# Optimization experiments

Measured on AMD Instinct MI355X. Metric: run time of the kernel, lower is better.

Reference implementation:

```python
import jax, jax.numpy as jnp
import numpy as np

B, S, D, H, V, C = 4, 2048, 1024, 16, 32000, 10
FFN_DIM = 2 * D
HD = D // H
SCALE = float(np.sqrt(HD))


def _posenc(seq, d):
    pos = jnp.arange(seq, dtype=jnp.float32)[:, None]
    div = jnp.exp(jnp.arange(0, d, 2, dtype=jnp.float32) * (-np.log(10000.0) / d))
    pe = jnp.zeros((seq, d), dtype=jnp.float32)
    pe = pe.at[:, 0::2].set(jnp.sin(pos * div))
    pe = pe.at[:, 1::2].set(jnp.cos(pos * div))
    return pe


def _layernorm(x, g, b, eps=1e-5):
    mu = jnp.mean(x, axis=-1, keepdims=True)
    var = jnp.mean(jnp.square(x - mu), axis=-1, keepdims=True)
    return (x - mu) * jax.lax.rsqrt(var + eps) * g + b


def setup_inputs() -> dict:
    key = jax.random.key(0)
    ks = jax.random.split(key, 10)
    x_ids = jax.random.randint(ks[0], (B, S), 0, V, dtype=jnp.int64 if jax.config.jax_enable_x64 else jnp.int32)
    mask = jnp.ones((B, S), dtype=jnp.int32)
    emb = (jax.random.normal(ks[1], (V, D), jnp.float32) * 0.02).at[0].set(0.0)  # padding_idx=0
    qkv_w = jax.random.normal(ks[2], (3 * D, D), jnp.float32) * 0.02
    fc_w = jax.random.normal(ks[3], (D, D), jnp.float32) * 0.02
    fc_b = jnp.zeros((D,), jnp.float32)
    ln1_g = jnp.ones((D,), jnp.float32); ln1_b = jnp.zeros((D,), jnp.float32)
    ffn_w1 = jax.random.normal(ks[4], (FFN_DIM, D), jnp.float32) * 0.02
    ffn_b1 = jnp.zeros((FFN_DIM,), jnp.float32)
    ffn_w2 = jax.random.normal(ks[5], (D, FFN_DIM), jnp.float32) * 0.02
    ffn_b2 = jnp.zeros((D,), jnp.float32)
    ln2_g = jnp.ones((D,), jnp.float32); ln2_b = jnp.zeros((D,), jnp.float32)
    pr_w1 = jax.random.normal(ks[6], (D, D), jnp.float32) * 0.02
    pr_b1 = jnp.zeros((D,), jnp.float32)
    pr_w2 = jax.random.normal(ks[7], (C, D), jnp.float32) * 0.02
    pr_b2 = jnp.zeros((C,), jnp.float32)
    return dict(x_ids=x_ids, mask=mask, emb=emb, qkv_w=qkv_w, fc_w=fc_w, fc_b=fc_b,
                ln1_g=ln1_g, ln1_b=ln1_b, ffn_w1=ffn_w1, ffn_b1=ffn_b1,
                ffn_w2=ffn_w2, ffn_b2=ffn_b2, ln2_g=ln2_g, ln2_b=ln2_b,
                pr_w1=pr_w1, pr_b1=pr_b1, pr_w2=pr_w2, pr_b2=pr_b2)


def reference(x_ids, mask, emb, qkv_w, fc_w, fc_b, ln1_g, ln1_b,
              ffn_w1, ffn_b1, ffn_w2, ffn_b2, ln2_g, ln2_b,
              pr_w1, pr_b1, pr_w2, pr_b2):
    # embedding + absolute positional encoding
    x = emb[x_ids] + _posenc(S, D)  # [B,S,D]
    residual = x
    # multi-head attention (dropout is identity at eval)
    qkv = jnp.einsum('bsd,ed->bse', x, qkv_w)  # [B,S,3D]
    q, k, v = jnp.split(qkv, 3, axis=-1)
    q = q.reshape(B, S, H, HD)
    k = k.reshape(B, S, H, HD)
    v = v.reshape(B, S, H, HD)
    attn = jnp.einsum('bqhd,bkhd->bhqk', q, k) / SCALE  # [B,H,S,S]
    attn = jnp.where(mask[:, None, None, :] == 0, -jnp.inf, attn)
    attn = jax.nn.softmax(attn, axis=-1)
    o = jnp.einsum('bhqk,bkhd->bqhd', attn, v).reshape(B, S, D)
    o = jnp.einsum('bsd,ed->bse', o, fc_w) + fc_b
    x = _layernorm(o + residual, ln1_g, ln1_b)
    # FFN block (residual + LayerNorm inside)
    h = jax.nn.gelu(jnp.einsum('bsd,fd->bsf', x, ffn_w1) + ffn_b1, approximate=False)
    h = jnp.einsum('bsf,df->bsd', h, ffn_w2) + ffn_b2
    x = _layernorm(h + x, ln2_g, ln2_b)
    # masked max-pool over sequence
    x = jnp.where(mask[:, :, None] == 0, -jnp.inf, x).max(axis=1)  # [B,D]
    # prediction head
    h = jax.nn.gelu(x @ pr_w1.T + pr_b1, approximate=False)
    logits = h @ pr_w2.T + pr_b2  # [B,C]
    return logits
```

## Files before the change

### kernel.cpp

```cpp
#include <hip/hip_runtime.h>
#include <math.h>

#define B_   4
#define S_   2048
#define D_   1024
#define H_   16
#define HD_  64
#define C_   10
#define FFN_ 2048
#define M_   (B_ * S_)
#define D3_  (3 * D_)

typedef unsigned short u16;
typedef __bf16 bf16x8 __attribute__((ext_vector_type(8)));
typedef float  f32x4  __attribute__((ext_vector_type(4)));

#define EXPSCL 0.18033688011112042f

__device__ __forceinline__ u16 f2bf(float f) {
  union { float f; unsigned u; } x; x.f = f;
  unsigned r = x.u + 0x7fffu + ((x.u >> 16) & 1u);
  return (u16)(r >> 16);
}
__device__ __forceinline__ unsigned cvtpk(float lo, float hi) {
  unsigned r;
  asm("v_cvt_pk_bf16_f32 %0, %1, %2" : "=v"(r) : "v"(lo), "v"(hi));
  return r;
}
__device__ __forceinline__ float gelu_f(float x) {
  return 0.5f * x * (1.f + erff(x * 0.70710678118654752440f));
}
__device__ __forceinline__ void gload_lds16(const void* g, void* l) {
  __builtin_amdgcn_global_load_lds(
      (const __attribute__((address_space(1))) unsigned int*)g,
      (__attribute__((address_space(3))) unsigned int*)l, 16, 0, 0);
}
__device__ __forceinline__ bf16x8 ldsfrag(const u16* buf, int rowbase, int fr, int kb) {
  return *(const bf16x8*)&buf[(rowbase + fr) * 64 + ((kb ^ (fr & 7)) << 3)];
}

#define CV0 786432
#define CV1 262144
#define CV2 524288
#define CV3 524288
__global__ __launch_bounds__(256) void cvt4_kernel(const float* __restrict__ s0,
                                                   const float* __restrict__ s1,
                                                   const float* __restrict__ s2,
                                                   const float* __restrict__ s3,
                                                   u16* __restrict__ d0,
                                                   u16* __restrict__ d1,
                                                   u16* __restrict__ d2,
                                                   u16* __restrict__ d3) {
  int v = blockIdx.x * 256 + threadIdx.x;
  const float* s; u16* d;
  if (v < CV0) { s = s0; d = d0; }
  else if (v < CV0 + CV1) { s = s1; d = d1; v -= CV0; }
  else if (v < CV0 + CV1 + CV2) { s = s2; d = d2; v -= CV0 + CV1; }
  else { s = s3; d = d3; v -= CV0 + CV1 + CV2; }
  const int i = v * 4;
  f32x4 x = *(const f32x4*)&s[i];
  ushort4 o;
  o.x = f2bf(x[0]); o.y = f2bf(x[1]); o.z = f2bf(x[2]); o.w = f2bf(x[3]);
  *(ushort4*)&d[i] = o;
}

__global__ __launch_bounds__(256) void embed_kernel(const int* __restrict__ ids,
                                                    const float* __restrict__ emb,
                                                    float* __restrict__ resid,
                                                    u16* __restrict__ xb) {
  const int m  = blockIdx.x;
  const int s  = m & (S_ - 1);
  const int id = ids[m];
  const int d0 = threadIdx.x * 4;
#pragma unroll
  for (int k = 0; k < 4; ++k) {
    const int d   = d0 + k;
    const float e = emb[(size_t)id * D_ + d];
    const float fr  = expf((float)(d & ~1) * (-9.210340371976184f / 1024.0f));
    const float ang = (float)s * fr;
    const float pe  = (d & 1) ? cosf(ang) : sinf(ang);
    const float v   = e + pe;
    resid[(size_t)m * D_ + d] = v;
    xb[(size_t)m * D_ + d]    = f2bf(v);
  }
}

template <int BIAS, int GELU, int OUTBF, int QSCALE>
__global__ __launch_bounds__(256) void gemm_bt(const u16* __restrict__ A,
                                               const u16* __restrict__ W,
                                               const float* __restrict__ bias,
                                               float* __restrict__ outf,
                                               u16* __restrict__ outb,
                                               int M, int N, int K) {
  __shared__ u16 As[128 * 64];
  __shared__ u16 Bs[128 * 64];
  const int tid  = threadIdx.x;
  const int lane = tid & 63;
  const int w    = tid >> 6;
  const int bx   = blockIdx.x, by = blockIdx.y;
  const int l3   = lane >> 3;
  const int sb   = (lane & 7) ^ l3;
  const u16* Ag0 = A + (size_t)(by * 128 + w * 32 + l3) * K + sb * 8;
  const u16* Wg0 = W + (size_t)(bx * 128 + w * 32 + l3) * K + sb * 8;

  f32x4 acc[4][4] = {};
  const int wr  = (w & 1) * 64;
  const int wc  = (w >> 1) * 64;
  const int fr  = lane & 15;
  const int fq  = lane >> 4;

  for (int kt = 0; kt < K; kt += 64) {
#pragma unroll
    for (int c = 0; c < 4; ++c) {
      gload_lds16(Ag0 + (size_t)(c * 8) * K + kt, &As[(w * 32 + c * 8) * 64]);
      gload_lds16(Wg0 + (size_t)(c * 8) * K + kt, &Bs[(w * 32 + c * 8) * 64]);
    }
    __syncthreads();
#pragma unroll
    for (int ks = 0; ks < 2; ++ks) {
      const int kb = ks * 4 + fq;
      bf16x8 af[4], bfr[4];
#pragma unroll
      for (int i = 0; i < 4; ++i) af[i] = ldsfrag(As, wr + i * 16, fr, kb);
#pragma unroll
      for (int j = 0; j < 4; ++j) bfr[j] = ldsfrag(Bs, wc + j * 16, fr, kb);
#pragma unroll
      for (int i = 0; i < 4; ++i)
#pragma unroll
        for (int j = 0; j < 4; ++j)
          acc[i][j] = __builtin_amdgcn_mfma_f32_16x16x32_bf16(bfr[j], af[i], acc[i][j], 0, 0, 0);
    }
    __syncthreads();
  }

  const float qs = (QSCALE && bx < 8) ? EXPSCL : 1.f;
#pragma unroll
  for (int i = 0; i < 4; ++i) {
    const int m = by * 128 + wr + i * 16 + fr;
#pragma unroll
    for (int j = 0; j < 4; ++j) {
      const int nb = bx * 128 + wc + j * 16 + fq * 4;
      f32x4 v = acc[i][j];
      if (BIAS) v += *(const f32x4*)&bias[nb];
      if (GELU) {
        v[0] = gelu_f(v[0]); v[1] = gelu_f(v[1]);
        v[2] = gelu_f(v[2]); v[3] = gelu_f(v[3]);
      }
      if (QSCALE) v *= qs;
      if (OUTBF) {
        ushort4 pk;
        pk.x = f2bf(v[0]); pk.y = f2bf(v[1]); pk.z = f2bf(v[2]); pk.w = f2bf(v[3]);
        *(ushort4*)&outb[(size_t)m * N + nb] = pk;
      } else {
        *(f32x4*)&outf[(size_t)m * N + nb] = v;
      }
    }
  }
}

__global__ __launch_bounds__(256) void vtrans_kernel(const u16* __restrict__ qkv,
                                                     u16* __restrict__ vt) {
  __shared__ u16 t[64 * 65];
  const int tid = threadIdx.x;
  const int st = blockIdx.x, h = blockIdx.y, b = blockIdx.z;
  {
    const int r = tid & 63, cg = tid >> 6;
    const u16* src = qkv + (size_t)(b * S_ + st * 64 + r) * D3_ + 2 * D_ + h * 64 + cg * 16;
    union { uint4 q; u16 s[8]; } a, c;
    a.q = *(const uint4*)src;
    c.q = *(const uint4*)(src + 8);
    u16* dl = &t[r * 65 + cg * 16];
#pragma unroll
    for (int k = 0; k < 8; ++k) { dl[k] = a.s[k]; dl[8 + k] = c.s[k]; }
  }
  __syncthreads();
  const int d = tid >> 2, sq = tid & 3;
  union { uint4 q[2]; u16 s[16]; } o;
#pragma unroll
  for (int k = 0; k < 16; ++k) o.s[k] = t[(sq * 16 + k) * 65 + d];
  u16* dst = vt + ((size_t)((b * H_ + h) * 64 + d)) * S_ + st * 64 + sq * 16;
  *(uint4*)dst = o.q[0];
  *(uint4*)(dst + 8) = o.q[1];
}

__global__ __launch_bounds__(256) void attn_mfma_kernel(const u16* __restrict__ qkv,
                                                        const u16* __restrict__ vt,
                                                        const int* __restrict__ mask,
                                                        u16* __restrict__ attno) {
  __shared__ u16 Ks[64 * 64];
  __shared__ u16 Vts[64 * 64];
  __shared__ u16 Ps[4][32 * 64];
  const int tid = threadIdx.x, lane = tid & 63, w = tid >> 6;
  const int qt = blockIdx.x, h = blockIdx.y, b = blockIdx.z;
  const int l3 = lane >> 3;
  const int sb = (lane & 7) ^ l3;
  const int fr = lane & 15, fq = lane >> 4;
  u16* PsFlat = &Ps[0][0];

  {
    const u16* qbase = qkv + (size_t)(b * S_ + qt * 128 + w * 32) * D3_ + h * 64 + sb * 8;
#pragma unroll
    for (int c = 0; c < 4; ++c)
      gload_lds16(qbase + (size_t)(c * 8 + l3) * D3_, &PsFlat[(w * 32 + c * 8) * 64]);
  }

  bool ALLV;
  {
    const int4* mp = (const int4*)&mask[b * S_];
    int mv = 1;
#pragma unroll
    for (int t = 0; t < 8; ++t) {
      const int4 m4 = mp[t * 64 + lane];
      mv &= (m4.x != 0) & (m4.y != 0) & (m4.z != 0) & (m4.w != 0);
    }
    ALLV = (__ballot(mv != 0) == ~0ull);
  }

  __syncthreads();

  bf16x8 qf[2][2];
#pragma unroll
  for (int ks = 0; ks < 2; ++ks)
#pragma unroll
    for (int i = 0; i < 2; ++i)
      qf[ks][i] = ldsfrag(PsFlat, w * 32 + i * 16, fr, ks * 4 + fq);

  __syncthreads();

  float l_st[2] = {0.f, 0.f};
  f32x4 ot[4][2] = {};
  u16* PsW = Ps[w];

  for (int kt = 0; kt < S_ / 64; ++kt) {
    {
      const u16* kbase = qkv + (size_t)(b * S_ + kt * 64 + w * 16) * D3_ + D_ + h * 64 + sb * 8;
      gload_lds16(kbase + (size_t)l3 * D3_, &Ks[(w * 16) * 64]);
      gload_lds16(kbase + (size_t)(8 + l3) * D3_, &Ks[(w * 16 + 8) * 64]);
      const u16* vbase = vt + ((size_t)((b * H_ + h) * 64 + w * 16)) * S_ + kt * 64 + sb * 8;
      gload_lds16(vbase + (size_t)l3 * S_, &Vts[(w * 16) * 64]);
      gload_lds16(vbase + (size_t)(8 + l3) * S_, &Vts[(w * 16 + 8) * 64]);
    }
    __syncthreads();

    f32x4 sf[4][2] = {};
#pragma unroll
    for (int ks = 0; ks < 2; ++ks) {
      const int kb = ks * 4 + fq;
      __builtin_amdgcn_s_setprio(1);
#pragma unroll
      for (int r4 = 0; r4 < 4; ++r4) {
        bf16x8 kf = ldsfrag(Ks, r4 * 16, fr, kb);
        sf[r4][0] = __builtin_amdgcn_mfma_f32_16x16x32_bf16(kf, qf[ks][0], sf[r4][0], 0, 0, 0);
        sf[r4][1] = __builtin_amdgcn_mfma_f32_16x16x32_bf16(kf, qf[ks][1], sf[r4][1], 0, 0, 0);
      }
      __builtin_amdgcn_s_setprio(0);
    }
    if (!ALLV) {
#pragma unroll
      for (int r4 = 0; r4 < 4; ++r4) {
        const int4 mm = *(const int4*)&mask[b * S_ + kt * 64 + r4 * 16 + fq * 4];
        f32x4 vb;
        vb[0] = mm.x ? 0.f : -1e30f;
        vb[1] = mm.y ? 0.f : -1e30f;
        vb[2] = mm.z ? 0.f : -1e30f;
        vb[3] = mm.w ? 0.f : -1e30f;
        sf[r4][0] += vb;
        sf[r4][1] += vb;
      }
    }

#pragma unroll
    for (int i = 0; i < 2; ++i) {
      const int prow = i * 16 + fr;
      u16* pw = PsW + prow * 64;
      float sum = l_st[i];
#pragma unroll
      for (int r4 = 0; r4 < 4; ++r4) {
        const float p0 = __builtin_exp2f(sf[r4][i][0]);
        const float p1 = __builtin_exp2f(sf[r4][i][1]);
        const float p2 = __builtin_exp2f(sf[r4][i][2]);
        const float p3 = __builtin_exp2f(sf[r4][i][3]);
        sum += (p0 + p1) + (p2 + p3);
        const int bk0 = 2 * r4 + (fq >> 1);
        const int off = ((bk0 ^ (prow & 7)) << 3) + ((fq & 1) << 2);
        uint2 pk; pk.x = cvtpk(p0, p1); pk.y = cvtpk(p2, p3);
        *(uint2*)&pw[off] = pk;
      }
      l_st[i] = sum;
    }
    asm volatile("s_waitcnt lgkmcnt(0)" ::: "memory");

#pragma unroll
    for (int ks = 0; ks < 2; ++ks) {
      const int kb = ks * 4 + fq;
      bf16x8 pf0 = ldsfrag(PsW, 0, fr, kb);
      bf16x8 pf1 = ldsfrag(PsW, 16, fr, kb);
      __builtin_amdgcn_s_setprio(1);
#pragma unroll
      for (int db = 0; db < 4; ++db) {
        bf16x8 vf = ldsfrag(Vts, db * 16, fr, kb);
        ot[db][0] = __builtin_amdgcn_mfma_f32_16x16x32_bf16(vf, pf0, ot[db][0], 0, 0, 0);
        ot[db][1] = __builtin_amdgcn_mfma_f32_16x16x32_bf16(vf, pf1, ot[db][1], 0, 0, 0);
      }
      __builtin_amdgcn_s_setprio(0);
    }
    __syncthreads();
  }

#pragma unroll
  for (int i = 0; i < 2; ++i) {
    float l = l_st[i];
    l += __shfl_xor(l, 16);
    l += __shfl_xor(l, 32);
    const float inv = (l > 0.f) ? 1.f / l : 0.f;
    const int qrow = qt * 128 + w * 32 + i * 16 + fr;
    u16* dst = attno + (size_t)(b * S_ + qrow) * D_ + h * 64 + fq * 4;
#pragma unroll
    for (int db = 0; db < 4; ++db) {
      ushort4 pk;
      pk.x = f2bf(ot[db][i][0] * inv);
      pk.y = f2bf(ot[db][i][1] * inv);
      pk.z = f2bf(ot[db][i][2] * inv);
      pk.w = f2bf(ot[db][i][3] * inv);
      *(ushort4*)&dst[db * 16] = pk;
    }
  }
}

template <int WRITEB>
__global__ __launch_bounds__(256) void ln_kernel(const float* __restrict__ a,
                                                 const float* __restrict__ res,
                                                 const float* __restrict__ g,
                                                 const float* __restrict__ be,
                                                 float* __restrict__ outf,
                                                 u16* __restrict__ outb) {
  const int row = blockIdx.x, tid = threadIdx.x;
  const int lane = tid & 63, w = tid >> 6;
  const size_t base = (size_t)row * D_ + tid * 4;
  const f32x4 va = *(const f32x4*)(a + base);
  const f32x4 vr = *(const f32x4*)(res + base);
  const f32x4 v  = va + vr;
  float s = v[0] + v[1] + v[2] + v[3];
#pragma unroll
  for (int o = 32; o > 0; o >>= 1) s += __shfl_xor(s, o);
  __shared__ float red[8];
  if (lane == 0) red[w] = s;
  __syncthreads();
  const float mu = (red[0] + red[1] + red[2] + red[3]) * (1.f / D_);
  const f32x4 d = v - mu;
  float s2 = d[0] * d[0] + d[1] * d[1] + d[2] * d[2] + d[3] * d[3];
#pragma unroll
  for (int o = 32; o > 0; o >>= 1) s2 += __shfl_xor(s2, o);
  if (lane == 0) red[4 + w] = s2;
  __syncthreads();
  const float var = (red[4] + red[5] + red[6] + red[7]) * (1.f / D_);
  const float rs = rsqrtf(var + 1e-5f);
  f32x4 y;
#pragma unroll
  for (int k = 0; k < 4; ++k) {
    const int ch = tid * 4 + k;
    y[k] = d[k] * rs * g[ch] + be[ch];
  }
  *(f32x4*)&outf[base] = y;
  if (WRITEB) {
    ushort4 pk;
    pk.x = f2bf(y[0]); pk.y = f2bf(y[1]); pk.z = f2bf(y[2]); pk.w = f2bf(y[3]);
    *(ushort4*)&outb[base] = pk;
  }
}

__global__ __launch_bounds__(256) void pool_part_kernel(const float* __restrict__ x,
                                                        const int* __restrict__ mask,
                                                        float* __restrict__ part) {
  const int b = blockIdx.y, ch = blockIdx.x;
  const int d0 = threadIdx.x * 4;
  f32x4 acc = {-INFINITY, -INFINITY, -INFINITY, -INFINITY};
  for (int ss = 0; ss < 64; ++ss) {
    const int s = ch * 64 + ss;
    if (mask[b * S_ + s] != 0) {
      const f32x4 v = *(const f32x4*)&x[(size_t)(b * S_ + s) * D_ + d0];
      acc[0] = fmaxf(acc[0], v[0]);
      acc[1] = fmaxf(acc[1], v[1]);
      acc[2] = fmaxf(acc[2], v[2]);
      acc[3] = fmaxf(acc[3], v[3]);
    }
  }
  *(f32x4*)&part[(size_t)(b * 32 + ch) * D_ + d0] = acc;
}
__global__ __launch_bounds__(256) void pool_final_kernel(const float* __restrict__ part,
                                                         float* __restrict__ pooled) {
  const int b = blockIdx.x;
  const int d0 = threadIdx.x * 4;
  f32x4 acc = {-INFINITY, -INFINITY, -INFINITY, -INFINITY};
  for (int ch = 0; ch < 32; ++ch) {
    const f32x4 v = *(const f32x4*)&part[(size_t)(b * 32 + ch) * D_ + d0];
    acc[0] = fmaxf(acc[0], v[0]);
    acc[1] = fmaxf(acc[1], v[1]);
    acc[2] = fmaxf(acc[2], v[2]);
    acc[3] = fmaxf(acc[3], v[3]);
  }
  *(f32x4*)&pooled[(size_t)b * D_ + d0] = acc;
}

__global__ __launch_bounds__(256) void head1_kernel(const float* __restrict__ pooled,
                                                    const float* __restrict__ w,
                                                    const float* __restrict__ bias,
                                                    float* __restrict__ hh) {
  const int lane = threadIdx.x & 63;
  const int gw = blockIdx.x * 4 + (threadIdx.x >> 6);
  const int b = gw >> 10, n = gw & 1023;
  const float* p  = pooled + b * 1024;
  const float* wr = w + (size_t)n * 1024;
  float s = 0.f;
  for (int d = lane; d < 1024; d += 64) s += p[d] * wr[d];
#pragma unroll
  for (int off = 32; off > 0; off >>= 1) s += __shfl_xor(s, off);
  if (lane == 0) hh[b * 1024 + n] = gelu_f(s + bias[n]);
}
__global__ __launch_bounds__(256) void head2_kernel(const float* __restrict__ hh,
                                                    const float* __restrict__ w,
                                                    const float* __restrict__ bias,
                                                    float* __restrict__ out) {
  const int lane = threadIdx.x & 63;
  const int gw = blockIdx.x * 4 + (threadIdx.x >> 6);
  const int b = gw / 10, c = gw % 10;
  const float* p  = hh + b * 1024;
  const float* wr = w + (size_t)c * 1024;
  float s = 0.f;
  for (int d = lane; d < 1024; d += 64) s += p[d] * wr[d];
#pragma unroll
  for (int off = 32; off > 0; off >>= 1) s += __shfl_xor(s, off);
  if (lane == 0) out[b * 10 + c] = s + bias[c];
}

#define OFF_RESID  0UL
#define OFF_F1     33554432UL
#define OFF_XB     67108864UL
#define OFF_QKVB   83886080UL
#define OFF_ATTNO  134217728UL
#define OFF_WQKV   150994944UL
#define OFF_WFC    157286400UL
#define OFF_WF1    159383552UL
#define OFF_WF2    163577856UL
#define OFF_PART   167772160UL
#define OFF_POOLED 168296448UL
#define OFF_HH     168312832UL

extern "C" void kernel_launch(void* const* d_in, const int* in_sizes, int n_in,
                              void* d_out, int out_size, void* d_ws, size_t ws_size,
                              hipStream_t stream) {
  const int*   x_ids  = (const int*)d_in[0];
  const int*   mask   = (const int*)d_in[1];
  const float* emb    = (const float*)d_in[2];
  const float* qkv_w  = (const float*)d_in[3];
  const float* fc_w   = (const float*)d_in[4];
  const float* fc_b   = (const float*)d_in[5];
  const float* ln1_g  = (const float*)d_in[6];
  const float* ln1_b  = (const float*)d_in[7];
  const float* ffn_w1 = (const float*)d_in[8];
  const float* ffn_b1 = (const float*)d_in[9];
  const float* ffn_w2 = (const float*)d_in[10];
  const float* ffn_b2 = (const float*)d_in[11];
  const float* ln2_g  = (const float*)d_in[12];
  const float* ln2_b  = (const float*)d_in[13];
  const float* pr_w1  = (const float*)d_in[14];
  const float* pr_b1  = (const float*)d_in[15];
  const float* pr_w2  = (const float*)d_in[16];
  const float* pr_b2  = (const float*)d_in[17];
  float* out = (float*)d_out;
  char* ws = (char*)d_ws;

  float* resid  = (float*)(ws + OFF_RESID);
  float* f1     = (float*)(ws + OFF_F1);
  u16*   vtb    = (u16*)(ws + OFF_F1);
  u16*   xb     = (u16*)(ws + OFF_XB);
  u16*   qkvb   = (u16*)(ws + OFF_QKVB);
  u16*   hb     = (u16*)(ws + OFF_QKVB);
  u16*   attnob = (u16*)(ws + OFF_ATTNO);
  u16*   wqkvb  = (u16*)(ws + OFF_WQKV);
  u16*   wfcb   = (u16*)(ws + OFF_WFC);
  u16*   wf1b   = (u16*)(ws + OFF_WF1);
  u16*   wf2b   = (u16*)(ws + OFF_WF2);
  float* part   = (float*)(ws + OFF_PART);
  float* pooled = (float*)(ws + OFF_POOLED);
  float* hh     = (float*)(ws + OFF_HH);

  cvt4_kernel<<<8192, 256, 0, stream>>>(qkv_w, fc_w, ffn_w1, ffn_w2,
                                        wqkvb, wfcb, wf1b, wf2b);

  embed_kernel<<<M_, 256, 0, stream>>>(x_ids, emb, resid, xb);

  gemm_bt<0, 0, 1, 1><<<dim3(D3_ / 128, M_ / 128), 256, 0, stream>>>(
      xb, wqkvb, nullptr, nullptr, qkvb, M_, D3_, D_);

  vtrans_kernel<<<dim3(S_ / 64, H_, B_), 256, 0, stream>>>(qkvb, vtb);

  attn_mfma_kernel<<<dim3(S_ / 128, H_, B_), 256, 0, stream>>>(qkvb, vtb, mask, attnob);

  gemm_bt<1, 0, 0, 0><<<dim3(D_ / 128, M_ / 128), 256, 0, stream>>>(
      attnob, wfcb, fc_b, f1, nullptr, M_, D_, D_);

  ln_kernel<1><<<M_, 256, 0, stream>>>(f1, resid, ln1_g, ln1_b, resid, xb);

  gemm_bt<1, 1, 1, 0><<<dim3(FFN_ / 128, M_ / 128), 256, 0, stream>>>(
      xb, wf1b, ffn_b1, nullptr, hb, M_, FFN_, D_);

  gemm_bt<1, 0, 0, 0><<<dim3(D_ / 128, M_ / 128), 256, 0, stream>>>(
      hb, wf2b, ffn_b2, f1, nullptr, M_, D_, FFN_);

  ln_kernel<0><<<M_, 256, 0, stream>>>(f1, resid, ln2_g, ln2_b, f1, nullptr);

  pool_part_kernel<<<dim3(32, B_), 256, 0, stream>>>(f1, mask, part);
  pool_final_kernel<<<B_, 256, 0, stream>>>(part, pooled);

  head1_kernel<<<1024, 256, 0, stream>>>(pooled, pr_w1, pr_b1, hh);
  head2_kernel<<<10, 256, 0, stream>>>(hh, pr_w2, pr_b2, out);
}
```

Baseline: 656.3 us.

## Remap workgroup IDs for XCD locality and vectorize embedding kernel

Workgroup indices in the GEMM and attention kernels are permuted so that consecutive tiles land on the same XCD. The aim is better L2 reuse of shared A/W rows and shared K/V heads across the MI355X chiplets. The embedding kernel is vectorized to float4 loads and stores, and it uses fast __expf/__sincosf to compute each sin/cos pair once. The remap assumes tile counts divisible by 8, and the fast intrinsics reduce positional-encoding accuracy slightly.

Measured after the change: 605.1 us. 7.8% less time.

```diff
diff --git a/kernel.cpp b/kernel.cpp
--- a/kernel.cpp
+++ b/kernel.cpp
@@ -72,17 +72,19 @@
   const int s  = m & (S_ - 1);
   const int id = ids[m];
   const int d0 = threadIdx.x * 4;
-#pragma unroll
-  for (int k = 0; k < 4; ++k) {
-    const int d   = d0 + k;
-    const float e = emb[(size_t)id * D_ + d];
-    const float fr  = expf((float)(d & ~1) * (-9.210340371976184f / 1024.0f));
-    const float ang = (float)s * fr;
-    const float pe  = (d & 1) ? cosf(ang) : sinf(ang);
-    const float v   = e + pe;
-    resid[(size_t)m * D_ + d] = v;
-    xb[(size_t)m * D_ + d]    = f2bf(v);
-  }
+  const f32x4 e = *(const f32x4*)&emb[(size_t)id * D_ + d0];
+  const float fs = (float)s;
+  const float f0 = __expf((float)d0 * (-9.210340371976184f / 1024.0f));
+  const float f1 = __expf((float)(d0 + 2) * (-9.210340371976184f / 1024.0f));
+  float s0, c0, s1, c1;
+  __sincosf(fs * f0, &s0, &c0);
+  __sincosf(fs * f1, &s1, &c1);
+  f32x4 v;
+  v[0] = e[0] + s0; v[1] = e[1] + c0; v[2] = e[2] + s1; v[3] = e[3] + c1;
+  *(f32x4*)&resid[(size_t)m * D_ + d0] = v;
+  ushort4 pk;
+  pk.x = f2bf(v[0]); pk.y = f2bf(v[1]); pk.z = f2bf(v[2]); pk.w = f2bf(v[3]);
+  *(ushort4*)&xb[(size_t)m * D_ + d0] = pk;
 }
 
 template <int BIAS, int GELU, int OUTBF, int QSCALE>
@@ -97,7 +99,11 @@
   const int tid  = threadIdx.x;
   const int lane = tid & 63;
   const int w    = tid >> 6;
-  const int bx   = blockIdx.x, by = blockIdx.y;
+  const int nx  = gridDim.x;
+  const int nwg = nx * gridDim.y;
+  int t = blockIdx.y * nx + blockIdx.x;
+  t = (t & 7) * (nwg >> 3) + (t >> 3);
+  const int bx = t % nx, by = t / nx;
   const int l3   = lane >> 3;
   const int sb   = (lane & 7) ^ l3;
   const u16* Ag0 = A + (size_t)(by * 128 + w * 32 + l3) * K + sb * 8;
@@ -191,7 +197,9 @@
   __shared__ u16 Vts[64 * 64];
   __shared__ u16 Ps[4][32 * 64];
   const int tid = threadIdx.x, lane = tid & 63, w = tid >> 6;
-  const int qt = blockIdx.x, h = blockIdx.y, b = blockIdx.z;
+  int t = (blockIdx.z * 16 + blockIdx.y) * 16 + blockIdx.x;
+  t = (t & 7) * 128 + (t >> 3);
+  const int qt = t & 15, h = (t >> 4) & 15, b = t >> 8;
   const int l3 = lane >> 3;
   const int sb = (lane & 7) ^ l3;
   const int fr = lane & 15, fq = lane >> 4;
@@ -209,8 +217,8 @@
     const int4* mp = (const int4*)&mask[b * S_];
     int mv = 1;
 #pragma unroll
-    for (int t = 0; t < 8; ++t) {
-      const int4 m4 = mp[t * 64 + lane];
+    for (int tt = 0; tt < 8; ++tt) {
+      const int4 m4 = mp[tt * 64 + lane];
       mv &= (m4.x != 0) & (m4.y != 0) & (m4.z != 0) & (m4.w != 0);
     }
     ALLV = (__ballot(mv != 0) == ~0ull);
```
